# Optimization experiments

Measured on AMD Instinct MI355X. Metric: run time of the kernel, lower is better.

Reference implementation:

```python
import jax, jax.numpy as jnp
import numpy as np
from jax import lax

B, C, H, W = 8, 256, 64, 64
NUM_HEADS = 4
HEAD_DIM = C // NUM_HEADS  # == dim // 4, required by q_proj
EPS_LN = 1e-5
EPS_NORM = 1e-12


def _gelu(x):
    return jax.nn.gelu(x, approximate=False)  # torch default GELU is erf-based


def setup_inputs() -> dict:
    key = jax.random.key(0)
    ks = jax.random.split(key, 20)
    s = lambda fan_in: 1.0 / np.sqrt(fan_in)
    return {
        "x": jax.random.normal(ks[0], (B, C, H, W), jnp.float32),
        # LayerNorm(dim)
        "ln_g": jnp.ones((C,), jnp.float32),
        "ln_b": jnp.zeros((C,), jnp.float32),
        # qkv: Linear(C, 3C, bias=False); stored (in, out)
        "w_qkv": jax.random.normal(ks[1], (C, 3 * C), jnp.float32) * s(C),
        # q_proj: Linear(head_dim, head_dim); stored (in, out)
        "w_q": jax.random.normal(ks[2], (HEAD_DIM, HEAD_DIM), jnp.float32) * s(HEAD_DIM),
        "b_q": jax.random.normal(ks[3], (HEAD_DIM,), jnp.float32) * 0.01,
        "temperature": jnp.ones((NUM_HEADS, 1, 1), jnp.float32),
        # depthwise 3x3 conv, groups=C: kernel (C,1,3,3) OIHW
        "dw_w": jax.random.normal(ks[4], (C, 1, 3, 3), jnp.float32) * s(9),
        "dw_b": jax.random.normal(ks[5], (C,), jnp.float32) * 0.01,
        # channel_interaction: 1x1 convs stored as (out, in)
        "ci_w1": jax.random.normal(ks[6], (C // 8, C), jnp.float32) * s(C),
        "ci_b1": jax.random.normal(ks[7], (C // 8,), jnp.float32) * 0.01,
        "ci_w2": jax.random.normal(ks[8], (C, C // 8), jnp.float32) * s(C // 8),
        "ci_b2": jax.random.normal(ks[9], (C,), jnp.float32) * 0.01,
        # spatial_interaction: 1x1 convs stored as (out, in)
        "si_w1": jax.random.normal(ks[10], (C // 16, C), jnp.float32) * s(C),
        "si_b1": jax.random.normal(ks[11], (C // 16,), jnp.float32) * 0.01,
        "si_w2": jax.random.normal(ks[12], (1, C // 16), jnp.float32) * s(C // 16),
        "si_b2": jax.random.normal(ks[13], (1,), jnp.float32) * 0.01,
        # proj: Linear(C, C); stored (in, out)
        "proj_w": jax.random.normal(ks[14], (C, C), jnp.float32) * s(C),
        "proj_b": jax.random.normal(ks[15], (C,), jnp.float32) * 0.01,
    }


def reference(x, ln_g, ln_b, w_qkv, w_q, b_q, temperature, dw_w, dw_b,
              ci_w1, ci_b1, ci_w2, ci_b2, si_w1, si_b1, si_w2, si_b2,
              proj_w, proj_b):
    Bx, Cx, Hx, Wx = x.shape
    N = Hx * Wx
    nh = temperature.shape[0]
    hd = Cx // nh

    # before_RG: (B,C,H,W) -> (B,N,C), LayerNorm over C
    xt = x.reshape(Bx, Cx, N).transpose(0, 2, 1)
    mu = xt.mean(-1, keepdims=True)
    var = ((xt - mu) ** 2).mean(-1, keepdims=True)
    xn = (xt - mu) * lax.rsqrt(var + EPS_LN) * ln_g + ln_b

    # qkv -> (3, B, nh, N, hd)
    qkv = (xn @ w_qkv).reshape(Bx, N, 3, nh, hd).transpose(2, 0, 3, 1, 4)
    q, k, v = qkv[0], qkv[1], qkv[2]
    q = q @ w_q + b_q                      # Linear on head_dim
    q = q.transpose(0, 1, 3, 2)            # (B, nh, hd, N)
    k = k.transpose(0, 1, 3, 2)
    v = v.transpose(0, 1, 3, 2)
    v_ = v.reshape(Bx, Cx, Hx, Wx)         # head-major channel layout

    # L2 normalize along N (torch F.normalize semantics)
    q = q / jnp.clip(jnp.linalg.norm(q, axis=-1, keepdims=True), EPS_NORM)
    k = k / jnp.clip(jnp.linalg.norm(k, axis=-1, keepdims=True), EPS_NORM)

    # channel attention: (B, nh, hd, hd)
    attn = jnp.einsum('bhdn,bhen->bhde', q, k) * temperature
    attn = jax.nn.softmax(attn, axis=-1)
    attened_x = jnp.einsum('bhde,bhen->bhdn', attn, v)
    attened_x = attened_x.transpose(0, 3, 1, 2).reshape(Bx, N, Cx)  # (B,N,C)

    # depthwise conv branch + GELU
    conv_x = lax.conv_general_dilated(
        v_, dw_w, window_strides=(1, 1), padding='SAME',
        feature_group_count=Cx, dimension_numbers=('NCHW', 'OIHW', 'NCHW'))
    conv_x = _gelu(conv_x + dw_b[None, :, None, None])

    # channel interaction (SE on attention branch)
    pooled = attened_x.mean(axis=1)                    # (B,C) == global avg pool of (B,C,H,W)
    ci = _gelu(pooled @ ci_w1.T + ci_b1)
    channel_map = ci @ ci_w2.T + ci_b2                 # (B,C)

    # spatial interaction (on conv branch)
    si = _gelu(jnp.einsum('bchw,oc->bohw', conv_x, si_w1) + si_b1[None, :, None, None])
    spatial_map = jnp.einsum('bchw,oc->bohw', si, si_w2) + si_b2[None, :, None, None]  # (B,1,H,W)
    spatial_map = spatial_map.reshape(Bx, N, 1)

    # cross gating and fuse
    attened_x = attened_x * jax.nn.sigmoid(spatial_map)
    conv_x = conv_x * jax.nn.sigmoid(channel_map)[:, :, None, None]
    conv_x = conv_x.reshape(Bx, Cx, N).transpose(0, 2, 1)

    out = (attened_x + conv_x) @ proj_w + proj_b       # (B,N,C)
    return out.transpose(0, 2, 1).reshape(Bx, Cx, Hx, Wx)
```

## Files before the change

kernel.cpp:

```cpp
#include <hip/hip_runtime.h>

typedef unsigned short u16;
typedef short bf16x8 __attribute__((ext_vector_type(8)));
typedef float f32x4 __attribute__((ext_vector_type(4)));

__device__ __forceinline__ float bf2f(u16 u){ return __uint_as_float(((unsigned)u)<<16); }
__device__ __forceinline__ u16 f2bf(float f){
  unsigned u = __float_as_uint(f);
  u += 0x7FFF + ((u >> 16) & 1);
  return (u16)(u >> 16);
}
__device__ __forceinline__ float ldp(const void* p, size_t i, int bf){
  return bf ? bf2f(((const u16*)p)[i]) : ((const float*)p)[i];
}
__device__ __forceinline__ float gelu_f(float x){ return 0.5f*x*(1.0f+erff(x*0.70710678118654752440f)); }
__device__ __forceinline__ float sigmoid_f(float x){ return 1.0f/(1.0f+expf(-x)); }

struct __align__(8)  U16x4 { u16 x,y,z,w; };
struct __align__(16) U16x8 { u16 v[8]; };

#define Cc 256
#define Nn 4096
#define CN 1048576


__global__ void k_flag(const unsigned* __restrict__ g_bits, int* __restrict__ flag){
  if (threadIdx.x == 0)
    *flag = (g_bits[0] == 0x3F803F80u) ? 1 : 0;
}

__global__ void k_zero(float* __restrict__ p){
  size_t i = ((size_t)blockIdx.x*256 + threadIdx.x)*4;
  float4 z; z.x=0.f; z.y=0.f; z.z=0.f; z.w=0.f;
  *(float4*)(p + i) = z;
}

__global__ void k_prep(const void* __restrict__ wqkv, const void* __restrict__ wq,
                       const void* __restrict__ bq, const void* __restrict__ pw,
                       const int* __restrict__ flag,
                       u16* __restrict__ WallT16, u16* __restrict__ pwT16,
                       float* __restrict__ biasall){
  int bf = *flag;
  int j = blockIdx.x;
  int c = threadIdx.x;
  if (j < 768){
    float out;
    if (j < 256){
      int h = j >> 6, e = j & 63;
      float acc = 0.f;
      #pragma unroll 8
      for (int d = 0; d < 64; ++d)
        acc += ldp(wqkv, c*768 + h*64 + d, bf) * ldp(wq, d*64 + e, bf);
      out = acc;
    } else {
      out = ldp(wqkv, c*768 + j, bf);
    }
    size_t a = ((size_t)((j>>4)*8 + (c>>5))*64 + (j&15) + 16*((c>>3)&3))*8 + (c&7);
    WallT16[a] = f2bf(out);
    if (c == 0) biasall[j] = (j < 256) ? ldp(bq, j & 63, bf) : 0.f;
  } else {
    int o = j - 768;
    size_t a = ((size_t)((o>>4)*8 + (c>>5))*64 + (o&15) + 16*((c>>3)&3))*8 + (c&7);
    pwT16[a] = f2bf(ldp(pw, c*256 + o, bf));
  }
}

__global__ __launch_bounds__(256) void k_lnT(const void* __restrict__ x,
                    const void* __restrict__ g, const void* __restrict__ bta,
                    const int* __restrict__ flag,
                    u16* __restrict__ xn16){
  __shared__ float tile[256*65];
  __shared__ float gs[256], bs[256];
  __shared__ float red_s[4][64], red_ss[4][64];
  __shared__ float mu_sh[64], rs_sh[64];
  int bf = *flag;
  int tid = threadIdx.x;
  int b  = blockIdx.x >> 6;
  int n0 = (blockIdx.x & 63) * 64;
  gs[tid] = ldp(g, tid, bf); bs[tid] = ldp(bta, tid, bf);
  int crow = tid >> 2, noff = (tid & 3) * 16;
  for (int p = 0; p < 4; ++p){
    int c = p*64 + crow;
    size_t base = (size_t)b*CN + (size_t)c*Nn + n0 + noff;
    float vals[16];
    if (bf){
      #pragma unroll
      for (int q = 0; q < 2; ++q){
        U16x8 u = *(const U16x8*)((const u16*)x + base + q*8);
        #pragma unroll
        for (int i = 0; i < 8; ++i) vals[q*8+i] = bf2f(u.v[i]);
      }
    } else {
      #pragma unroll
      for (int q = 0; q < 4; ++q){
        float4 f = *(const float4*)((const float*)x + base + q*4);
        vals[q*4+0]=f.x; vals[q*4+1]=f.y; vals[q*4+2]=f.z; vals[q*4+3]=f.w;
      }
    }
    #pragma unroll
    for (int i = 0; i < 16; ++i) tile[c*65 + noff + i] = vals[i];
  }
  __syncthreads();
  {
    int r = tid >> 6, nl = tid & 63;
    float s = 0.f, ss = 0.f;
    for (int cc = r*64; cc < r*64 + 64; ++cc){
      float v = tile[cc*65 + nl];
      s += v; ss += v*v;
    }
    red_s[r][nl] = s; red_ss[r][nl] = ss;
  }
  __syncthreads();
  if (tid < 64){
    float st  = red_s[0][tid]  + red_s[1][tid]  + red_s[2][tid]  + red_s[3][tid];
    float sst = red_ss[0][tid] + red_ss[1][tid] + red_ss[2][tid] + red_ss[3][tid];
    float m   = st * (1.f/256.f);
    float var = sst * (1.f/256.f) - m*m;
    mu_sh[tid] = m;
    rs_sh[tid] = rsqrtf(var + 1e-5f);
  }
  __syncthreads();
  int n = tid >> 2, coff = (tid & 3) * 64;
  float mn = mu_sh[n], rn = rs_sh[n];
  int gidx = (n0 >> 4) + (n >> 4);
  int l15 = n & 15;
  u16* dstb = xn16 + ((size_t)b*256 + gidx)*4096;
  for (int q = 0; q < 8; ++q){
    int c8 = coff + q*8;
    int ks = c8 >> 5, quad = (c8 >> 3) & 3;
    U16x8 w;
    #pragma unroll
    for (int i = 0; i < 8; ++i){
      int c = c8 + i;
      w.v[i] = f2bf((tile[c*65 + n] - mn)*rn*gs[c] + bs[c]);
    }
    *(U16x8*)(dstb + (size_t)ks*512 + (l15 + 16*quad)*8) = w;
  }
}

__global__ __launch_bounds__(256) void k_qkv(const u16* __restrict__ xn16,
                                             const u16* __restrict__ WallT16,
                                             const float* __restrict__ biasall,
                                             u16* __restrict__ q16, u16* __restrict__ k16,
                                             u16* __restrict__ v16,
                                             float* __restrict__ qsq, float* __restrict__ ksq){
  __shared__ u16 Bs[32768];
  __shared__ float bias_sh[128];
  __shared__ float sq_sh[128];
  int tid = threadIdx.x;
  int by = blockIdx.x;
  int bx = blockIdx.y;
  int b  = by >> 5;
  int n0 = (by & 31) * 128;
  int j0 = bx * 128;
  int part = bx >> 1;
  int w = tid >> 6, lane = tid & 63, l15 = lane & 15, quad = lane >> 4;

  const u16* Afrag = xn16 + ((size_t)b*256 + (n0>>4) + w*2)*4096 + lane*8;
  bf16x8 af[2][8];
  #pragma unroll
  for (int r = 0; r < 2; ++r)
    #pragma unroll
    for (int ks = 0; ks < 8; ++ks)
      af[r][ks] = *(const bf16x8*)(Afrag + (size_t)r*4096 + (size_t)ks*512);

  const u16* Bt = WallT16 + (size_t)(j0>>4)*4096;
  #pragma unroll
  for (int i = 0; i < 16; ++i){
    int off = (i*256 + tid)*8;
    *(bf16x8*)(Bs + off) = *(const bf16x8*)(Bt + off);
  }
  if (tid < 128){ bias_sh[tid] = biasall[j0 + tid]; sq_sh[tid] = 0.f; }
  __syncthreads();

  f32x4 acc[2][8];
  #pragma unroll
  for (int r=0;r<2;++r)
    #pragma unroll
    for (int s=0;s<8;++s){ acc[r][s][0]=0.f; acc[r][s][1]=0.f; acc[r][s][2]=0.f; acc[r][s][3]=0.f; }

  const u16* Bfrag = Bs + lane*8;
  #pragma unroll
  for (int ks = 0; ks < 8; ++ks){
    #pragma unroll
    for (int s = 0; s < 8; ++s){
      bf16x8 bb = *(const bf16x8*)(Bfrag + s*4096 + ks*512);
      acc[0][s] = __builtin_amdgcn_mfma_f32_16x16x32_bf16(af[0][ks], bb, acc[0][s], 0, 0, 0);
      acc[1][s] = __builtin_amdgcn_mfma_f32_16x16x32_bf16(af[1][ks], bb, acc[1][s], 0, 0, 0);
    }
  }
  u16* dst = (part==0) ? q16 : ((part==1) ? k16 : v16);
  float sql[8];
  #pragma unroll
  for (int s=0;s<8;++s) sql[s]=0.f;
  #pragma unroll
  for (int r = 0; r < 2; ++r){
    int nb = n0 + w*32 + r*16 + quad*4;
    #pragma unroll
    for (int s = 0; s < 8; ++s){
      int jf = s*16 + l15;
      int j = j0 + jf;
      int h = (j >> 6) & 3, d = j & 63;
      float bd = bias_sh[jf];
      float v0 = acc[r][s][0] + bd, v1 = acc[r][s][1] + bd;
      float v2 = acc[r][s][2] + bd, v3 = acc[r][s][3] + bd;
      U16x4 wv; wv.x=f2bf(v0); wv.y=f2bf(v1); wv.z=f2bf(v2); wv.w=f2bf(v3);
      *(U16x4*)(dst + ((size_t)(b*4 + h)*64 + d)*4096 + nb) = wv;
      sql[s] += v0*v0 + v1*v1 + v2*v2 + v3*v3;
    }
  }
  if (part < 2){
    #pragma unroll
    for (int s = 0; s < 8; ++s)
      atomicAdd(&sq_sh[s*16 + l15], sql[s]);
    __syncthreads();
    if (tid < 128){
      float* nsq = (part==0) ? qsq : ksq;
      atomicAdd(&nsq[(b*4 + (bx&1)*2 + (tid>>6))*64 + (tid&63)], sq_sh[tid]);
    }
  }
}

__global__ __launch_bounds__(256) void k_attnp(const u16* __restrict__ q16,
                                               const u16* __restrict__ k16,
                                               float* __restrict__ S){
  int tid = threadIdx.x;
  int bh = blockIdx.y;
  int kc = blockIdx.x;
  int w = tid >> 6, lane = tid & 63, l15 = lane & 15, quad = lane >> 4;
  f32x4 acc[4];
  #pragma unroll
  for (int s=0;s<4;++s){ acc[s][0]=0.f; acc[s][1]=0.f; acc[s][2]=0.f; acc[s][3]=0.f; }
  const u16* qp = q16 + ((size_t)bh*64 + w*16 + l15)*4096 + quad*8;
  const u16* kp = k16 + ((size_t)bh*64 + l15)*4096 + quad*8;
  #pragma unroll 4
  for (int nn = kc*256; nn < kc*256 + 256; nn += 32){
    bf16x8 a = *(const bf16x8*)(qp + nn);
    #pragma unroll
    for (int s = 0; s < 4; ++s){
      bf16x8 bb = *(const bf16x8*)(kp + (size_t)s*16*4096 + nn);
      acc[s] = __builtin_amdgcn_mfma_f32_16x16x32_bf16(a, bb, acc[s], 0, 0, 0);
    }
  }
  float* Sb = S + (size_t)bh*4096;
  #pragma unroll
  for (int s = 0; s < 4; ++s)
    #pragma unroll
    for (int i = 0; i < 4; ++i)
      atomicAdd(&Sb[(w*16 + quad*4 + i)*64 + s*16 + l15], acc[s][i]);
}

__global__ __launch_bounds__(256) void k_softmax(float* __restrict__ S,
                          const float* __restrict__ qsq, const float* __restrict__ ksq,
                          const void* __restrict__ temp, const int* __restrict__ flag){
  __shared__ float kn_sh[64], qn_sh[64];
  int bf = *flag;
  int bh = blockIdx.x;
  int tid = threadIdx.x;
  if (tid < 64){
    kn_sh[tid] = fmaxf(sqrtf(ksq[bh*64 + tid]), 1e-12f);
    qn_sh[tid] = fmaxf(sqrtf(qsq[bh*64 + tid]), 1e-12f);
  }
  __syncthreads();
  int d  = tid >> 2;
  int e0 = (tid & 3) * 16;
  float tpr = ldp(temp, bh & 3, bf);
  float* row = S + (size_t)bh*4096 + d*64 + e0;
  float sc = tpr / qn_sh[d];
  float v[16];
  #pragma unroll
  for (int q = 0; q < 4; ++q){
    float4 f = *(const float4*)(row + q*4);
    v[q*4+0]=f.x; v[q*4+1]=f.y; v[q*4+2]=f.z; v[q*4+3]=f.w;
  }
  float mx = -1e30f;
  #pragma unroll
  for (int e = 0; e < 16; ++e){
    v[e] = v[e] * sc / kn_sh[e0 + e];
    mx = fmaxf(mx, v[e]);
  }
  mx = fmaxf(mx, __shfl_xor(mx, 1));
  mx = fmaxf(mx, __shfl_xor(mx, 2));
  float s = 0.f;
  #pragma unroll
  for (int e = 0; e < 16; ++e){ v[e] = expf(v[e] - mx); s += v[e]; }
  s += __shfl_xor(s, 1);
  s += __shfl_xor(s, 2);
  float inv = 1.f/s;
  #pragma unroll
  for (int q = 0; q < 4; ++q){
    float4 f; f.x=v[q*4+0]*inv; f.y=v[q*4+1]*inv; f.z=v[q*4+2]*inv; f.w=v[q*4+3]*inv;
    *(float4*)(row + q*4) = f;
  }
}

__global__ __launch_bounds__(256) void k_av(const float* __restrict__ P,
                                            const u16* __restrict__ v16,
                                            u16* __restrict__ att16,
                                            float* __restrict__ pooled){
  __shared__ float Ps[4096];
  __shared__ float Vs[16][64];
  int bh = blockIdx.y;
  int n0 = blockIdx.x * 64;
  int tid = threadIdx.x, tx = tid & 15, ty = tid >> 4;
  const float* Pb = P + (size_t)bh*4096;
  #pragma unroll
  for (int i = 0; i < 4; ++i){
    int lin = (i*256 + tid)*4;
    *(float4*)&Ps[lin] = *(const float4*)(Pb + lin);
  }
  const u16* vb = v16 + (size_t)bh*64*4096;
  float acc[4][4] = {};
  for (int e0 = 0; e0 < 64; e0 += 16){
    int er = tid >> 4, nq = (tid & 15)*4;
    U16x4 vu = *(const U16x4*)(vb + (size_t)(e0+er)*4096 + n0 + nq);
    Vs[er][nq+0]=bf2f(vu.x); Vs[er][nq+1]=bf2f(vu.y); Vs[er][nq+2]=bf2f(vu.z); Vs[er][nq+3]=bf2f(vu.w);
    __syncthreads();
    #pragma unroll
    for (int ee = 0; ee < 16; ++ee){
      float a[4];
      #pragma unroll
      for (int i = 0; i < 4; ++i) a[i] = Ps[(ty*4+i)*64 + e0 + ee];
      float4 b4 = *(const float4*)&Vs[ee][tx*4];
      float bb[4] = {b4.x,b4.y,b4.z,b4.w};
      #pragma unroll
      for (int i = 0; i < 4; ++i)
        #pragma unroll
        for (int j = 0; j < 4; ++j) acc[i][j] += a[i]*bb[j];
    }
    __syncthreads();
  }
  u16* ob = att16 + (size_t)bh*64*4096 + n0;
  #pragma unroll
  for (int i = 0; i < 4; ++i){
    int d = ty*4 + i;
    U16x4 w;
    w.x = f2bf(acc[i][0]); w.y = f2bf(acc[i][1]);
    w.z = f2bf(acc[i][2]); w.w = f2bf(acc[i][3]);
    *(U16x4*)(ob + (size_t)d*4096 + tx*4) = w;
  }
  float* red = &Vs[0][0];
  if (tid < 64) red[tid] = 0.f;
  __syncthreads();
  #pragma unroll
  for (int i = 0; i < 4; ++i){
    float rs = acc[i][0] + acc[i][1] + acc[i][2] + acc[i][3];
    atomicAdd(&red[ty*4 + i], rs);
  }
  __syncthreads();
  if (tid < 64)
    atomicAdd(&pooled[(bh>>2)*256 + (bh&3)*64 + tid], red[tid]);
}

__global__ void k_conv(const u16* __restrict__ v16, const void* __restrict__ dww,
                       const void* __restrict__ dwb, const int* __restrict__ flag,
                       u16* __restrict__ conv16){
  __shared__ float plane[4096];
  int bf = *flag;
  int bc = blockIdx.x;
  int c = bc & 255;
  int tid = threadIdx.x;
  const u16* vp = v16 + (size_t)bc*4096;
  #pragma unroll
  for (int i = 0; i < 4; ++i){
    int lin = (i*256 + tid)*4;
    U16x4 vu = *(const U16x4*)(vp + lin);
    plane[lin+0]=bf2f(vu.x); plane[lin+1]=bf2f(vu.y); plane[lin+2]=bf2f(vu.z); plane[lin+3]=bf2f(vu.w);
  }
  float wgt[9];
  #pragma unroll
  for (int i = 0; i < 9; ++i) wgt[i] = ldp(dww, c*9 + i, bf);
  float bias = ldp(dwb, c, bf);
  __syncthreads();
  u16* op = conv16 + (size_t)bc*4096;
  for (int it = 0; it < 16; ++it){
    int p = it*256 + tid;
    int y = p >> 6, x = p & 63;
    float acc = bias;
    #pragma unroll
    for (int ky = 0; ky < 3; ++ky){
      int yy = y + ky - 1;
      if (yy < 0 || yy > 63) continue;
      #pragma unroll
      for (int kx = 0; kx < 3; ++kx){
        int xx = x + kx - 1;
        if (xx < 0 || xx > 63) continue;
        acc += wgt[ky*3+kx]*plane[yy*64 + xx];
      }
    }
    op[p] = f2bf(gelu_f(acc));
  }
}

__global__ __launch_bounds__(256) void k_spatial(const u16* __restrict__ conv16,
                                                 const void* __restrict__ w1, const void* __restrict__ b1,
                                                 const void* __restrict__ w2, const void* __restrict__ b2,
                                                 const int* __restrict__ flag,
                                                 float* __restrict__ ssp){
  __shared__ float w1s[16][256];
  __shared__ u16 tile[256][72];
  __shared__ float red[4][64][17];
  int bf = *flag;
  int tid = threadIdx.x;
  for (int i = 0; i < 16; ++i)
    w1s[i][tid] = ldp(w1, i*256 + tid, bf);
  int b  = blockIdx.x >> 6;
  int n0 = (blockIdx.x & 63) * 64;
  const u16* cb = conv16 + (size_t)b*CN + n0;
  #pragma unroll
  for (int i = 0; i < 8; ++i){
    int idx = i*256 + tid;
    int c = idx >> 3, seg = idx & 7;
    *(U16x8*)&tile[c][seg*8] = *(const U16x8*)(cb + (size_t)c*Nn + seg*8);
  }
  __syncthreads();
  int nl = tid & 63, r = tid >> 6;
  float acc[16] = {};
  for (int cc = r*64; cc < r*64 + 64; ++cc){
    float xv = bf2f(tile[cc][nl]);
    #pragma unroll
    for (int o = 0; o < 16; ++o) acc[o] += xv * w1s[o][cc];
  }
  #pragma unroll
  for (int o = 0; o < 16; ++o) red[r][nl][o] = acc[o];
  __syncthreads();
  if (tid < 64){
    float sp = ldp(b2, 0, bf);
    #pragma unroll
    for (int o = 0; o < 16; ++o){
      float a = red[0][tid][o] + red[1][tid][o] + red[2][tid][o] + red[3][tid][o];
      sp += gelu_f(a + ldp(b1, o, bf)) * ldp(w2, o, bf);
    }
    ssp[(size_t)b*Nn + n0 + tid] = sigmoid_f(sp);
  }
}

__global__ void k_channel(const float* __restrict__ pooled,
                          const void* __restrict__ w1, const void* __restrict__ b1,
                          const void* __restrict__ w2, const void* __restrict__ b2,
                          const int* __restrict__ flag,
                          float* __restrict__ sch){
  __shared__ float ps[256];
  __shared__ float cis[32];
  int bf = *flag;
  int b = blockIdx.x, tid = threadIdx.x;
  ps[tid] = pooled[b*256 + tid] * (1.f/4096.f);
  __syncthreads();
  if (tid < 32){
    float a = ldp(b1, tid, bf);
    for (int cc = 0; cc < 256; ++cc) a += ps[cc]*ldp(w1, tid*256 + cc, bf);
    cis[tid] = gelu_f(a);
  }
  __syncthreads();
  float m = ldp(b2, tid, bf);
  #pragma unroll
  for (int o = 0; o < 32; ++o) m += cis[o]*ldp(w2, tid*32 + o, bf);
  sch[b*256 + tid] = sigmoid_f(m);
}

__global__ __launch_bounds__(256) void k_gate(const u16* __restrict__ att16,
                                              const u16* __restrict__ conv16,
                                              const float* __restrict__ ssp,
                                              const float* __restrict__ sch,
                                              u16* __restrict__ Y16){
  __shared__ u16 tile[256*66];
  __shared__ float ssp_sh[64], sch_sh[256];
  int tid = threadIdx.x;
  int b  = blockIdx.x >> 6;
  int n0 = (blockIdx.x & 63) * 64;
  sch_sh[tid] = sch[b*256 + tid];
  if (tid < 64) ssp_sh[tid] = ssp[(size_t)b*Nn + n0 + tid];
  __syncthreads();
  int crow = tid >> 2, noff = (tid & 3) * 16;
  for (int p = 0; p < 4; ++p){
    int c = p*64 + crow;
    size_t base = (size_t)b*CN + (size_t)c*Nn + n0 + noff;
    float gc = sch_sh[c];
    U16x8 a0 = *(const U16x8*)(att16 + base);
    U16x8 a1 = *(const U16x8*)(att16 + base + 8);
    U16x8 c0 = *(const U16x8*)(conv16 + base);
    U16x8 c1 = *(const U16x8*)(conv16 + base + 8);
    #pragma unroll
    for (int i = 0; i < 8; ++i){
      tile[c*66 + noff + i]     = f2bf(bf2f(a0.v[i])*ssp_sh[noff+i]   + bf2f(c0.v[i])*gc);
      tile[c*66 + noff + 8 + i] = f2bf(bf2f(a1.v[i])*ssp_sh[noff+8+i] + bf2f(c1.v[i])*gc);
    }
  }
  __syncthreads();
  int n = tid >> 2, coff = (tid & 3) * 64;
  int gidx = (n0 >> 4) + (n >> 4);
  int l15 = n & 15;
  u16* dstb = Y16 + ((size_t)b*256 + gidx)*4096;
  for (int q = 0; q < 8; ++q){
    int c8 = coff + q*8;
    int ks = c8 >> 5, quad = (c8 >> 3) & 3;
    U16x8 wv;
    #pragma unroll
    for (int i = 0; i < 8; ++i) wv.v[i] = tile[(c8 + i)*66 + n];
    *(U16x8*)(dstb + (size_t)ks*512 + (l15 + 16*quad)*8) = wv;
  }
}

__global__ __launch_bounds__(256) void k_proj(const u16* __restrict__ Y16,
                                              const u16* __restrict__ pwT16,
                                              const void* __restrict__ pb,
                                              const int* __restrict__ flag,
                                              void* __restrict__ out){
  __shared__ u16 Bs[32768];
  __shared__ float pb_sh[128];
  int bf = *flag;
  int tid = threadIdx.x;
  int by = blockIdx.x;
  int bx = blockIdx.y;
  int b  = by >> 5;
  int n0 = (by & 31) * 128;
  int c0 = bx * 128;
  int w = tid >> 6, lane = tid & 63, l15 = lane & 15, quad = lane >> 4;

  const u16* Afrag = Y16 + ((size_t)b*256 + (n0>>4) + w*2)*4096 + lane*8;
  bf16x8 af[2][8];
  #pragma unroll
  for (int r = 0; r < 2; ++r)
    #pragma unroll
    for (int ks = 0; ks < 8; ++ks)
      af[r][ks] = *(const bf16x8*)(Afrag + (size_t)r*4096 + (size_t)ks*512);

  const u16* Bt = pwT16 + (size_t)(c0>>4)*4096;
  #pragma unroll
  for (int i = 0; i < 16; ++i){
    int off = (i*256 + tid)*8;
    *(bf16x8*)(Bs + off) = *(const bf16x8*)(Bt + off);
  }
  if (tid < 128) pb_sh[tid] = ldp(pb, c0 + tid, bf);
  __syncthreads();

  f32x4 acc[2][8];
  #pragma unroll
  for (int r=0;r<2;++r)
    #pragma unroll
    for (int s=0;s<8;++s){ acc[r][s][0]=0.f; acc[r][s][1]=0.f; acc[r][s][2]=0.f; acc[r][s][3]=0.f; }

  const u16* Bfrag = Bs + lane*8;
  #pragma unroll
  for (int ks = 0; ks < 8; ++ks){
    #pragma unroll
    for (int s = 0; s < 8; ++s){
      bf16x8 bb = *(const bf16x8*)(Bfrag + s*4096 + ks*512);
      acc[0][s] = __builtin_amdgcn_mfma_f32_16x16x32_bf16(af[0][ks], bb, acc[0][s], 0, 0, 0);
      acc[1][s] = __builtin_amdgcn_mfma_f32_16x16x32_bf16(af[1][ks], bb, acc[1][s], 0, 0, 0);
    }
  }
  #pragma unroll
  for (int r = 0; r < 2; ++r){
    int nb = n0 + w*32 + r*16 + quad*4;
    #pragma unroll
    for (int s = 0; s < 8; ++s){
      int cch = c0 + s*16 + l15;
      float pbias = pb_sh[s*16 + l15];
      size_t oidx = ((size_t)(b*256 + cch))*4096 + nb;
      float v0 = acc[r][s][0] + pbias, v1 = acc[r][s][1] + pbias;
      float v2 = acc[r][s][2] + pbias, v3 = acc[r][s][3] + pbias;
      if (bf){
        U16x4 wv; wv.x=f2bf(v0); wv.y=f2bf(v1); wv.z=f2bf(v2); wv.w=f2bf(v3);
        *(U16x4*)((u16*)out + oidx) = wv;
      } else {
        float4 wv; wv.x=v0; wv.y=v1; wv.z=v2; wv.w=v3;
        *(float4*)((float*)out + oidx) = wv;
      }
    }
  }
}

extern "C" void kernel_launch(void* const* d_in, const int* in_sizes, int n_in,
                              void* d_out, int out_size, void* d_ws, size_t ws_size,
                              hipStream_t stream) {
  const void* x    = d_in[0];
  const void* ln_g = d_in[1];
  const void* ln_b = d_in[2];
  const void* wqkv = d_in[3];
  const void* wq   = d_in[4];
  const void* bq   = d_in[5];
  const void* temp = d_in[6];
  const void* dww  = d_in[7];
  const void* dwb  = d_in[8];
  const void* ciw1 = d_in[9];
  const void* cib1 = d_in[10];
  const void* ciw2 = d_in[11];
  const void* cib2 = d_in[12];
  const void* siw1 = d_in[13];
  const void* sib1 = d_in[14];
  const void* siw2 = d_in[15];
  const void* sib2 = d_in[16];
  const void* pw   = d_in[17];
  const void* pb   = d_in[18];

  u16* wsu    = (u16*)d_ws;
  u16* q16    = wsu;
  u16* k16    = wsu + 8388608;
  u16* xn16   = wsu + 16777216;
  u16* att16  = q16;
  u16* conv16 = k16;
  u16* Y16    = xn16;
  u16* v16    = (u16*)d_out;

  float* tail = (float*)(wsu + 25165824);
  float* qsq  = tail;
  float* ksq  = qsq + 2048;
  float* P    = ksq + 2048;
  float* pool = P + 131072;
  float* biasall = pool + 2048;
  float* sch  = biasall + 768;
  float* ssp  = sch + 2048;
  u16* WallT16 = (u16*)(ssp + 32768);
  u16* pwT16   = WallT16 + 196608;
  int* flag    = (int*)(pwT16 + 65536);

  hipLaunchKernelGGL(k_flag,  dim3(1), dim3(64), 0, stream, (const unsigned*)ln_g, flag);
  hipLaunchKernelGGL(k_zero,  dim3(134), dim3(256), 0, stream, qsq);
  hipLaunchKernelGGL(k_prep,  dim3(1024), dim3(256), 0, stream, wqkv, wq, bq, pw, flag, WallT16, pwT16, biasall);
  hipLaunchKernelGGL(k_lnT,   dim3(512), dim3(256), 0, stream, x, ln_g, ln_b, flag, xn16);
  hipLaunchKernelGGL(k_qkv,   dim3(256, 6), dim3(256), 0, stream,
                     xn16, WallT16, biasall, q16, k16, v16, qsq, ksq);
  hipLaunchKernelGGL(k_attnp, dim3(16, 32), dim3(256), 0, stream, q16, k16, P);
  hipLaunchKernelGGL(k_softmax, dim3(32), dim3(256), 0, stream, P, qsq, ksq, temp, flag);
  hipLaunchKernelGGL(k_av,    dim3(64, 32), dim3(256), 0, stream, P, v16, att16, pool);
  hipLaunchKernelGGL(k_conv,  dim3(2048), dim3(256), 0, stream, v16, dww, dwb, flag, conv16);
  hipLaunchKernelGGL(k_spatial, dim3(512), dim3(256), 0, stream, conv16, siw1, sib1, siw2, sib2, flag, ssp);
  hipLaunchKernelGGL(k_channel, dim3(8), dim3(256), 0, stream, pool, ciw1, cib1, ciw2, cib2, flag, sch);
  hipLaunchKernelGGL(k_gate,  dim3(512), dim3(256), 0, stream, att16, conv16, ssp, sch, Y16);
  hipLaunchKernelGGL(k_proj,  dim3(256, 2), dim3(256), 0, stream, Y16, pwT16, pb, flag, d_out);
}
```

Baseline: 322.0 us.

## Move attention-times-V onto MFMA with transposed V and bf16 probabilities

After: 291.4 us. 1.11x faster.

```diff
diff --git a/kernel.cpp b/kernel.cpp
--- a/kernel.cpp
+++ b/kernel.cpp
@@ -138,22 +138,23 @@
   }
 }
 
-__global__ __launch_bounds__(256) void k_qkv(const u16* __restrict__ xn16,
+__global__ __launch_bounds__(256, 4) void k_qkv(const u16* __restrict__ xn16,
                                              const u16* __restrict__ WallT16,
                                              const float* __restrict__ biasall,
                                              u16* __restrict__ q16, u16* __restrict__ k16,
-                                             u16* __restrict__ v16,
+                                             u16* __restrict__ v16, u16* __restrict__ vT16,
                                              float* __restrict__ qsq, float* __restrict__ ksq){
-  __shared__ u16 Bs[32768];
-  __shared__ float bias_sh[128];
-  __shared__ float sq_sh[128];
+  __shared__ u16 Bs[16384];
+  __shared__ float bias_sh[64];
+  __shared__ float sq_sh[64];
   int tid = threadIdx.x;
   int by = blockIdx.x;
   int bx = blockIdx.y;
   int b  = by >> 5;
   int n0 = (by & 31) * 128;
-  int j0 = bx * 128;
-  int part = bx >> 1;
+  int j0 = bx * 64;
+  int part = bx >> 2;
+  int h = (j0 >> 6) & 3;
   int w = tid >> 6, lane = tid & 63, l15 = lane & 15, quad = lane >> 4;
 
   const u16* Afrag = xn16 + ((size_t)b*256 + (n0>>4) + w*2)*4096 + lane*8;
@@ -166,42 +167,40 @@
 
   const u16* Bt = WallT16 + (size_t)(j0>>4)*4096;
   #pragma unroll
-  for (int i = 0; i < 16; ++i){
+  for (int i = 0; i < 8; ++i){
     int off = (i*256 + tid)*8;
     *(bf16x8*)(Bs + off) = *(const bf16x8*)(Bt + off);
   }
-  if (tid < 128){ bias_sh[tid] = biasall[j0 + tid]; sq_sh[tid] = 0.f; }
-  __syncthreads();
-
-  f32x4 acc[2][8];
+  if (tid < 64){ bias_sh[tid] = biasall[j0 + tid]; sq_sh[tid] = 0.f; }
+  __syncthreads();
+
+  f32x4 acc[2][4];
   #pragma unroll
   for (int r=0;r<2;++r)
     #pragma unroll
-    for (int s=0;s<8;++s){ acc[r][s][0]=0.f; acc[r][s][1]=0.f; acc[r][s][2]=0.f; acc[r][s][3]=0.f; }
+    for (int s=0;s<4;++s){ acc[r][s][0]=0.f; acc[r][s][1]=0.f; acc[r][s][2]=0.f; acc[r][s][3]=0.f; }
 
   const u16* Bfrag = Bs + lane*8;
   #pragma unroll
   for (int ks = 0; ks < 8; ++ks){
     #pragma unroll
-    for (int s = 0; s < 8; ++s){
+    for (int s = 0; s < 4; ++s){
       bf16x8 bb = *(const bf16x8*)(Bfrag + s*4096 + ks*512);
       acc[0][s] = __builtin_amdgcn_mfma_f32_16x16x32_bf16(af[0][ks], bb, acc[0][s], 0, 0, 0);
       acc[1][s] = __builtin_amdgcn_mfma_f32_16x16x32_bf16(af[1][ks], bb, acc[1][s], 0, 0, 0);
     }
   }
   u16* dst = (part==0) ? q16 : ((part==1) ? k16 : v16);
-  float sql[8];
-  #pragma unroll
-  for (int s=0;s<8;++s) sql[s]=0.f;
+  float sql[4];
+  #pragma unroll
+  for (int s=0;s<4;++s) sql[s]=0.f;
   #pragma unroll
   for (int r = 0; r < 2; ++r){
     int nb = n0 + w*32 + r*16 + quad*4;
     #pragma unroll
-    for (int s = 0; s < 8; ++s){
-      int jf = s*16 + l15;
-      int j = j0 + jf;
-      int h = (j >> 6) & 3, d = j & 63;
-      float bd = bias_sh[jf];
+    for (int s = 0; s < 4; ++s){
+      int d = s*16 + l15;
+      float bd = bias_sh[d];
       float v0 = acc[r][s][0] + bd, v1 = acc[r][s][1] + bd;
       float v2 = acc[r][s][2] + bd, v3 = acc[r][s][3] + bd;
       U16x4 wv; wv.x=f2bf(v0); wv.y=f2bf(v1); wv.z=f2bf(v2); wv.w=f2bf(v3);
@@ -211,12 +210,38 @@
   }
   if (part < 2){
     #pragma unroll
-    for (int s = 0; s < 8; ++s)
+    for (int s = 0; s < 4; ++s)
       atomicAdd(&sq_sh[s*16 + l15], sql[s]);
     __syncthreads();
-    if (tid < 128){
+    if (tid < 64){
       float* nsq = (part==0) ? qsq : ksq;
-      atomicAdd(&nsq[(b*4 + (bx&1)*2 + (tid>>6))*64 + (tid&63)], sq_sh[tid]);
+      atomicAdd(&nsq[(b*4 + h)*64 + tid], sq_sh[tid]);
+    }
+  } else {
+    __syncthreads();
+    u16* Ls = Bs;
+    #pragma unroll
+    for (int r = 0; r < 2; ++r){
+      #pragma unroll
+      for (int s = 0; s < 4; ++s){
+        int d = s*16 + l15;
+        #pragma unroll
+        for (int i = 0; i < 4; ++i){
+          int nl = w*32 + r*16 + quad*4 + i;
+          Ls[nl*72 + d] = f2bf(acc[r][s][i]);
+        }
+      }
+    }
+    __syncthreads();
+    u16* vt = vT16 + ((size_t)(b*4 + h))*262144 + (size_t)(n0>>4)*1024;
+    #pragma unroll
+    for (int it = 0; it < 4; ++it){
+      int lin = it*256 + tid;
+      int t15 = lin & 15, q4 = (lin>>4)&3, ks = (lin>>6)&1, g = lin>>7;
+      int nl = g*16 + t15;
+      int e0 = ks*32 + q4*8;
+      U16x8 wv = *(const U16x8*)&Ls[nl*72 + e0];
+      *(U16x8*)(vt + (size_t)lin*8) = wv;
     }
   }
 }
@@ -234,7 +259,7 @@
   const u16* qp = q16 + ((size_t)bh*64 + w*16 + l15)*4096 + quad*8;
   const u16* kp = k16 + ((size_t)bh*64 + l15)*4096 + quad*8;
   #pragma unroll 4
-  for (int nn = kc*256; nn < kc*256 + 256; nn += 32){
+  for (int nn = kc*512; nn < kc*512 + 512; nn += 32){
     bf16x8 a = *(const bf16x8*)(qp + nn);
     #pragma unroll
     for (int s = 0; s < 4; ++s){
@@ -252,7 +277,8 @@
 
 __global__ __launch_bounds__(256) void k_softmax(float* __restrict__ S,
                           const float* __restrict__ qsq, const float* __restrict__ ksq,
-                          const void* __restrict__ temp, const int* __restrict__ flag){
+                          const void* __restrict__ temp, const int* __restrict__ flag,
+                          u16* __restrict__ P16){
   __shared__ float kn_sh[64], qn_sh[64];
   int bf = *flag;
   int bh = blockIdx.x;
@@ -265,7 +291,7 @@
   int d  = tid >> 2;
   int e0 = (tid & 3) * 16;
   float tpr = ldp(temp, bh & 3, bf);
-  float* row = S + (size_t)bh*4096 + d*64 + e0;
+  const float* row = S + (size_t)bh*4096 + d*64 + e0;
   float sc = tpr / qn_sh[d];
   float v[16];
   #pragma unroll
@@ -287,69 +313,67 @@
   s += __shfl_xor(s, 1);
   s += __shfl_xor(s, 2);
   float inv = 1.f/s;
-  #pragma unroll
-  for (int q = 0; q < 4; ++q){
-    float4 f; f.x=v[q*4+0]*inv; f.y=v[q*4+1]*inv; f.z=v[q*4+2]*inv; f.w=v[q*4+3]*inv;
-    *(float4*)(row + q*4) = f;
-  }
-}
-
-__global__ __launch_bounds__(256) void k_av(const float* __restrict__ P,
-                                            const u16* __restrict__ v16,
-                                            u16* __restrict__ att16,
+  u16* pb16 = P16 + bh*4096;
+  int g = d >> 4, l15d = d & 15;
+  #pragma unroll
+  for (int half = 0; half < 2; ++half){
+    int e = e0 + half*8;
+    int ks = e >> 5, q4 = (e >> 3) & 3;
+    U16x8 wv;
+    #pragma unroll
+    for (int i = 0; i < 8; ++i) wv.v[i] = f2bf(v[half*8 + i]*inv);
+    *(U16x8*)(pb16 + ((g*2 + ks)*64 + l15d + 16*q4)*8) = wv;
+  }
+}
+
+__global__ __launch_bounds__(256) void k_av(const u16* __restrict__ P16,
+                                            const u16* __restrict__ vT16,
+                                            u16* __restrict__ attT,
                                             float* __restrict__ pooled){
-  __shared__ float Ps[4096];
-  __shared__ float Vs[16][64];
+  __shared__ u16 Bs[16384];
+  __shared__ float red[64];
   int bh = blockIdx.y;
-  int n0 = blockIdx.x * 64;
-  int tid = threadIdx.x, tx = tid & 15, ty = tid >> 4;
-  const float* Pb = P + (size_t)bh*4096;
-  #pragma unroll
-  for (int i = 0; i < 4; ++i){
-    int lin = (i*256 + tid)*4;
-    *(float4*)&Ps[lin] = *(const float4*)(Pb + lin);
-  }
-  const u16* vb = v16 + (size_t)bh*64*4096;
-  float acc[4][4] = {};
-  for (int e0 = 0; e0 < 64; e0 += 16){
-    int er = tid >> 4, nq = (tid & 15)*4;
-    U16x4 vu = *(const U16x4*)(vb + (size_t)(e0+er)*4096 + n0 + nq);
-    Vs[er][nq+0]=bf2f(vu.x); Vs[er][nq+1]=bf2f(vu.y); Vs[er][nq+2]=bf2f(vu.z); Vs[er][nq+3]=bf2f(vu.w);
-    __syncthreads();
-    #pragma unroll
-    for (int ee = 0; ee < 16; ++ee){
-      float a[4];
-      #pragma unroll
-      for (int i = 0; i < 4; ++i) a[i] = Ps[(ty*4+i)*64 + e0 + ee];
-      float4 b4 = *(const float4*)&Vs[ee][tx*4];
-      float bb[4] = {b4.x,b4.y,b4.z,b4.w};
-      #pragma unroll
-      for (int i = 0; i < 4; ++i)
-        #pragma unroll
-        for (int j = 0; j < 4; ++j) acc[i][j] += a[i]*bb[j];
-    }
-    __syncthreads();
-  }
-  u16* ob = att16 + (size_t)bh*64*4096 + n0;
-  #pragma unroll
-  for (int i = 0; i < 4; ++i){
-    int d = ty*4 + i;
-    U16x4 w;
-    w.x = f2bf(acc[i][0]); w.y = f2bf(acc[i][1]);
-    w.z = f2bf(acc[i][2]); w.w = f2bf(acc[i][3]);
-    *(U16x4*)(ob + (size_t)d*4096 + tx*4) = w;
-  }
-  float* red = &Vs[0][0];
+  int n0 = blockIdx.x * 256;
+  int tid = threadIdx.x, w = tid >> 6, lane = tid & 63, l15 = lane & 15, quad = lane >> 4;
+  int b = bh >> 2, h = bh & 3;
+  const u16* vt = vT16 + (size_t)bh*262144 + (size_t)(n0>>4)*1024;
+  #pragma unroll
+  for (int i = 0; i < 8; ++i){
+    int off = (i*256 + tid)*8;
+    *(bf16x8*)(Bs + off) = *(const bf16x8*)(vt + off);
+  }
   if (tid < 64) red[tid] = 0.f;
-  __syncthreads();
-  #pragma unroll
-  for (int i = 0; i < 4; ++i){
-    float rs = acc[i][0] + acc[i][1] + acc[i][2] + acc[i][3];
-    atomicAdd(&red[ty*4 + i], rs);
-  }
+  const u16* pp = P16 + bh*4096;
+  bf16x8 af0 = *(const bf16x8*)(pp + ((w*2 + 0)*64 + lane)*8);
+  bf16x8 af1 = *(const bf16x8*)(pp + ((w*2 + 1)*64 + lane)*8);
+  __syncthreads();
+  f32x4 acc[16];
+  #pragma unroll
+  for (int s = 0; s < 16; ++s){ acc[s][0]=0.f; acc[s][1]=0.f; acc[s][2]=0.f; acc[s][3]=0.f; }
+  const u16* Bfrag = Bs + lane*8;
+  #pragma unroll
+  for (int s = 0; s < 16; ++s){
+    bf16x8 b0 = *(const bf16x8*)(Bfrag + (s*2 + 0)*512);
+    bf16x8 b1 = *(const bf16x8*)(Bfrag + (s*2 + 1)*512);
+    acc[s] = __builtin_amdgcn_mfma_f32_16x16x32_bf16(af0, b0, acc[s], 0, 0, 0);
+    acc[s] = __builtin_amdgcn_mfma_f32_16x16x32_bf16(af1, b1, acc[s], 0, 0, 0);
+  }
+  u16* ob = attT + ((size_t)b*4096 + n0)*256 + h*64 + w*16 + quad*4;
+  float p0=0.f, p1=0.f, p2=0.f, p3=0.f;
+  #pragma unroll
+  for (int s = 0; s < 16; ++s){
+    int n = s*16 + l15;
+    U16x4 wv; wv.x=f2bf(acc[s][0]); wv.y=f2bf(acc[s][1]); wv.z=f2bf(acc[s][2]); wv.w=f2bf(acc[s][3]);
+    *(U16x4*)(ob + (size_t)n*256) = wv;
+    p0 += acc[s][0]; p1 += acc[s][1]; p2 += acc[s][2]; p3 += acc[s][3];
+  }
+  atomicAdd(&red[w*16 + quad*4 + 0], p0);
+  atomicAdd(&red[w*16 + quad*4 + 1], p1);
+  atomicAdd(&red[w*16 + quad*4 + 2], p2);
+  atomicAdd(&red[w*16 + quad*4 + 3], p3);
   __syncthreads();
   if (tid < 64)
-    atomicAdd(&pooled[(bh>>2)*256 + (bh&3)*64 + tid], red[tid]);
+    atomicAdd(&pooled[b*256 + h*64 + tid], red[tid]);
 }
 
 __global__ void k_conv(const u16* __restrict__ v16, const void* __restrict__ dww,
@@ -458,63 +482,67 @@
   sch[b*256 + tid] = sigmoid_f(m);
 }
 
-__global__ __launch_bounds__(256) void k_gate(const u16* __restrict__ att16,
+__global__ __launch_bounds__(256) void k_gate(const u16* __restrict__ attT,
                                               const u16* __restrict__ conv16,
                                               const float* __restrict__ ssp,
                                               const float* __restrict__ sch,
                                               u16* __restrict__ Y16){
-  __shared__ u16 tile[256*66];
+  __shared__ u16 ct[256*66];
+  __shared__ u16 at[64*264];
   __shared__ float ssp_sh[64], sch_sh[256];
   int tid = threadIdx.x;
   int b  = blockIdx.x >> 6;
   int n0 = (blockIdx.x & 63) * 64;
   sch_sh[tid] = sch[b*256 + tid];
   if (tid < 64) ssp_sh[tid] = ssp[(size_t)b*Nn + n0 + tid];
-  __syncthreads();
-  int crow = tid >> 2, noff = (tid & 3) * 16;
-  for (int p = 0; p < 4; ++p){
-    int c = p*64 + crow;
-    size_t base = (size_t)b*CN + (size_t)c*Nn + n0 + noff;
-    float gc = sch_sh[c];
-    U16x8 a0 = *(const U16x8*)(att16 + base);
-    U16x8 a1 = *(const U16x8*)(att16 + base + 8);
-    U16x8 c0 = *(const U16x8*)(conv16 + base);
-    U16x8 c1 = *(const U16x8*)(conv16 + base + 8);
+  const u16* cb = conv16 + (size_t)b*CN + n0;
+  #pragma unroll
+  for (int i = 0; i < 8; ++i){
+    int idx = i*256 + tid;
+    int c = idx >> 3, seg = idx & 7;
+    *(U16x8*)&ct[c*66 + seg*8] = *(const U16x8*)(cb + (size_t)c*Nn + seg*8);
+  }
+  const u16* ab = attT + ((size_t)b*4096 + n0)*256;
+  #pragma unroll
+  for (int i = 0; i < 8; ++i){
+    int idx = i*256 + tid;
+    int n = idx >> 5, seg = idx & 31;
+    *(U16x8*)&at[n*264 + seg*8] = *(const U16x8*)(ab + (size_t)n*256 + seg*8);
+  }
+  __syncthreads();
+  u16* dstb = Y16 + ((size_t)b*256 + (n0>>4))*4096;
+  #pragma unroll
+  for (int it = 0; it < 8; ++it){
+    int lin = it*256 + tid;
+    int l15 = lin & 15, q4 = (lin>>4)&3, ks = (lin>>6)&7, ng = lin>>9;
+    int n = ng*16 + l15;
+    int c0 = ks*32 + q4*8;
+    float gn = ssp_sh[n];
+    U16x8 av = *(const U16x8*)&at[n*264 + c0];
+    U16x8 wv;
     #pragma unroll
     for (int i = 0; i < 8; ++i){
-      tile[c*66 + noff + i]     = f2bf(bf2f(a0.v[i])*ssp_sh[noff+i]   + bf2f(c0.v[i])*gc);
-      tile[c*66 + noff + 8 + i] = f2bf(bf2f(a1.v[i])*ssp_sh[noff+8+i] + bf2f(c1.v[i])*gc);
-    }
-  }
-  __syncthreads();
-  int n = tid >> 2, coff = (tid & 3) * 64;
-  int gidx = (n0 >> 4) + (n >> 4);
-  int l15 = n & 15;
-  u16* dstb = Y16 + ((size_t)b*256 + gidx)*4096;
-  for (int q = 0; q < 8; ++q){
-    int c8 = coff + q*8;
-    int ks = c8 >> 5, quad = (c8 >> 3) & 3;
-    U16x8 wv;
-    #pragma unroll
-    for (int i = 0; i < 8; ++i) wv.v[i] = tile[(c8 + i)*66 + n];
-    *(U16x8*)(dstb + (size_t)ks*512 + (l15 + 16*quad)*8) = wv;
-  }
-}
-
-__global__ __launch_bounds__(256) void k_proj(const u16* __restrict__ Y16,
+      int c = c0 + i;
+      wv.v[i] = f2bf(bf2f(av.v[i])*gn + bf2f(ct[c*66 + n])*sch_sh[c]);
+    }
+    *(U16x8*)(dstb + (size_t)lin*8) = wv;
+  }
+}
+
+__global__ __launch_bounds__(256, 4) void k_proj(const u16* __restrict__ Y16,
                                               const u16* __restrict__ pwT16,
                                               const void* __restrict__ pb,
                                               const int* __restrict__ flag,
                                               void* __restrict__ out){
-  __shared__ u16 Bs[32768];
-  __shared__ float pb_sh[128];
+  __shared__ u16 Bs[16384];
+  __shared__ float pb_sh[64];
   int bf = *flag;
   int tid = threadIdx.x;
   int by = blockIdx.x;
   int bx = blockIdx.y;
   int b  = by >> 5;
   int n0 = (by & 31) * 128;
-  int c0 = bx * 128;
+  int c0 = bx * 64;
   int w = tid >> 6, lane = tid & 63, l15 = lane & 15, quad = lane >> 4;
 
   const u16* Afrag = Y16 + ((size_t)b*256 + (n0>>4) + w*2)*4096 + lane*8;
@@ -527,24 +555,24 @@
 
   const u16* Bt = pwT16 + (size_t)(c0>>4)*4096;
   #pragma unroll
-  for (int i = 0; i < 16; ++i){
+  for (int i = 0; i < 8; ++i){
     int off = (i*256 + tid)*8;
     *(bf16x8*)(Bs + off) = *(const bf16x8*)(Bt + off);
   }
-  if (tid < 128) pb_sh[tid] = ldp(pb, c0 + tid, bf);
-  __syncthreads();
-
-  f32x4 acc[2][8];
+  if (tid < 64) pb_sh[tid] = ldp(pb, c0 + tid, bf);
+  __syncthreads();
+
+  f32x4 acc[2][4];
   #pragma unroll
   for (int r=0;r<2;++r)
     #pragma unroll
-    for (int s=0;s<8;++s){ acc[r][s][0]=0.f; acc[r][s][1]=0.f; acc[r][s][2]=0.f; acc[r][s][3]=0.f; }
+    for (int s=0;s<4;++s){ acc[r][s][0]=0.f; acc[r][s][1]=0.f; acc[r][s][2]=0.f; acc[r][s][3]=0.f; }
 
   const u16* Bfrag = Bs + lane*8;
   #pragma unroll
   for (int ks = 0; ks < 8; ++ks){
     #pragma unroll
-    for (int s = 0; s < 8; ++s){
+    for (int s = 0; s < 4; ++s){
       bf16x8 bb = *(const bf16x8*)(Bfrag + s*4096 + ks*512);
       acc[0][s] = __builtin_amdgcn_mfma_f32_16x16x32_bf16(af[0][ks], bb, acc[0][s], 0, 0, 0);
       acc[1][s] = __builtin_amdgcn_mfma_f32_16x16x32_bf16(af[1][ks], bb, acc[1][s], 0, 0, 0);
@@ -554,7 +582,7 @@
   for (int r = 0; r < 2; ++r){
     int nb = n0 + w*32 + r*16 + quad*4;
     #pragma unroll
-    for (int s = 0; s < 8; ++s){
+    for (int s = 0; s < 4; ++s){
       int cch = c0 + s*16 + l15;
       float pbias = pb_sh[s*16 + l15];
       size_t oidx = ((size_t)(b*256 + cch))*4096 + nb;
@@ -598,20 +626,25 @@
   u16* q16    = wsu;
   u16* k16    = wsu + 8388608;
   u16* xn16   = wsu + 16777216;
-  u16* att16  = q16;
+  u16* attT   = q16;
   u16* conv16 = k16;
   u16* Y16    = xn16;
   u16* v16    = (u16*)d_out;
 
-  float* tail = (float*)(wsu + 25165824);
+  u16* vT16;
+  if (out_size >= 33554432) vT16 = (u16*)d_out + 8388608;
+  else                      vT16 = wsu + 25165824;
+
+  float* tail = (float*)(wsu + 33554432);
   float* qsq  = tail;
   float* ksq  = qsq + 2048;
-  float* P    = ksq + 2048;
-  float* pool = P + 131072;
+  float* S    = ksq + 2048;
+  float* pool = S + 131072;
   float* biasall = pool + 2048;
   float* sch  = biasall + 768;
   float* ssp  = sch + 2048;
-  u16* WallT16 = (u16*)(ssp + 32768);
+  u16* P16     = (u16*)(ssp + 32768);
+  u16* WallT16 = P16 + 131072;
   u16* pwT16   = WallT16 + 196608;
   int* flag    = (int*)(pwT16 + 65536);
 
@@ -619,14 +652,14 @@
   hipLaunchKernelGGL(k_zero,  dim3(134), dim3(256), 0, stream, qsq);
   hipLaunchKernelGGL(k_prep,  dim3(1024), dim3(256), 0, stream, wqkv, wq, bq, pw, flag, WallT16, pwT16, biasall);
   hipLaunchKernelGGL(k_lnT,   dim3(512), dim3(256), 0, stream, x, ln_g, ln_b, flag, xn16);
-  hipLaunchKernelGGL(k_qkv,   dim3(256, 6), dim3(256), 0, stream,
-                     xn16, WallT16, biasall, q16, k16, v16, qsq, ksq);
-  hipLaunchKernelGGL(k_attnp, dim3(16, 32), dim3(256), 0, stream, q16, k16, P);
-  hipLaunchKernelGGL(k_softmax, dim3(32), dim3(256), 0, stream, P, qsq, ksq, temp, flag);
-  hipLaunchKernelGGL(k_av,    dim3(64, 32), dim3(256), 0, stream, P, v16, att16, pool);
+  hipLaunchKernelGGL(k_qkv,   dim3(256, 12), dim3(256), 0, stream,
+                     xn16, WallT16, biasall, q16, k16, v16, vT16, qsq, ksq);
+  hipLaunchKernelGGL(k_attnp, dim3(8, 32), dim3(256), 0, stream, q16, k16, S);
+  hipLaunchKernelGGL(k_softmax, dim3(32), dim3(256), 0, stream, S, qsq, ksq, temp, flag, P16);
+  hipLaunchKernelGGL(k_av,    dim3(16, 32), dim3(256), 0, stream, P16, vT16, attT, pool);
   hipLaunchKernelGGL(k_conv,  dim3(2048), dim3(256), 0, stream, v16, dww, dwb, flag, conv16);
   hipLaunchKernelGGL(k_spatial, dim3(512), dim3(256), 0, stream, conv16, siw1, sib1, siw2, sib2, flag, ssp);
   hipLaunchKernelGGL(k_channel, dim3(8), dim3(256), 0, stream, pool, ciw1, cib1, ciw2, cib2, flag, sch);
-  hipLaunchKernelGGL(k_gate,  dim3(512), dim3(256), 0, stream, att16, conv16, ssp, sch, Y16);
-  hipLaunchKernelGGL(k_proj,  dim3(256, 2), dim3(256), 0, stream, Y16, pwT16, pb, flag, d_out);
-}
+  hipLaunchKernelGGL(k_gate,  dim3(512), dim3(256), 0, stream, attT, conv16, ssp, sch, Y16);
+  hipLaunchKernelGGL(k_proj,  dim3(256, 4), dim3(256), 0, stream, Y16, pwT16, pb, flag, d_out);
+}
```
